# Performance work log

Measured on AMD Instinct MI355X. Metric: run time of the kernel, lower is better.

## Reference

```python
import jax, jax.numpy as jnp
import numpy as np

_EPS = 1e-12      # degenerate-triangle denominator guard
_CHUNK = 64       # triangles processed per scan step


def _bary(p, a, b, c):
    """Barycentric coords of points p w.r.t. triangle (a,b,c). Broadcasts.
    Returns [..., 3] = (u, v, w); -1 everywhere for degenerate triangles."""
    v0 = b - a
    v1 = c - a
    v2 = p - a
    d00 = jnp.sum(v0 * v0, -1)
    d01 = jnp.sum(v0 * v1, -1)
    d11 = jnp.sum(v1 * v1, -1)
    d20 = jnp.sum(v2 * v0, -1)
    d21 = jnp.sum(v2 * v1, -1)
    denom = d00 * d11 - d01 * d01
    bad = jnp.abs(denom) < _EPS
    ds = jnp.where(bad, 1.0, denom)
    v = (d11 * d20 - d01 * d21) / ds
    w = (d00 * d21 - d01 * d20) / ds
    u = 1.0 - v - w
    bar = jnp.stack([u, v, w], -1)
    return jnp.where(bad[..., None], -1.0, bar)


def _pixel_grid(res):
    # pixel-center UVs; x = u along columns, y = v along rows
    t = (jnp.arange(res, dtype=jnp.float32) + 0.5) / res
    gy, gx = jnp.meshgrid(t, t, indexing='ij')
    return jnp.stack([gx, gy], -1)  # [res, res, 2]


def _rasterize_ids(uv, face_indices, res):
    """For each bake pixel, the index of the first (lowest-index) triangle
    containing it, or -1 (== rast[...,-1] in the slang kernel)."""
    px = _pixel_grid(res)                    # [H, W, 2]
    tri = uv[face_indices]                   # [Nf, 3, 2]
    nf = tri.shape[0]
    nchunk = nf // _CHUNK
    tri_c = tri[: nchunk * _CHUNK].reshape(nchunk, _CHUNK, 3, 2)
    fid0 = jnp.full((res, res), -1, dtype=jnp.int32)

    def step(fid, xs):
        ci, tc = xs                          # tc: [C, 3, 2]
        bar = _bary(px[:, :, None, :], tc[:, 0], tc[:, 1], tc[:, 2])  # [H, W, C, 3]
        inside = jnp.all(bar >= 0.0, axis=-1)                          # [H, W, C]
        hit = jnp.any(inside, axis=-1)
        first = jnp.argmax(inside, axis=-1).astype(jnp.int32)          # first hit in chunk
        cand = ci * _CHUNK + first
        fid = jnp.where(hit & (fid < 0), cand, fid)
        return fid, None

    fid, _ = jax.lax.scan(step, fid0, (jnp.arange(nchunk, dtype=jnp.int32), tri_c))
    return fid


def _interpolate(attr, uv, face_indices, fid, res):
    px = _pixel_grid(res)
    tri_idx = face_indices[jnp.clip(fid, 0)]        # [H, W, 3] vertex ids of hit face
    verts = uv[tri_idx]                             # [H, W, 3, 2]
    bar = _bary(px, verts[..., 0, :], verts[..., 1, :], verts[..., 2, :])  # [H, W, 3]
    av = attr[tri_idx]                              # [H, W, 3, 3]
    out = jnp.einsum('hwk,hwkc->hwc', bar, av)
    return jnp.where(fid[..., None] >= 0, out, 0.0)  # zeros outside coverage (kernel inits output to 0)


def setup_inputs() -> dict:
    key = jax.random.key(0)
    k1, k2, k3 = jax.random.split(key, 3)
    Nv, Nf, res = 50000, 512, 512
    attr = jax.random.normal(k1, (Nv, 3), dtype=jnp.float32)
    uv = jax.random.uniform(k2, (Nv, 2), dtype=jnp.float32)
    face_indices = jax.random.randint(k3, (Nf, 3), 0, Nv, dtype=jnp.int32)
    return {"attr": attr, "uv": uv, "face_indices": face_indices, "bake_resolution": res}


def reference(attr, uv, face_indices, bake_resolution):
    fid = _rasterize_ids(uv, face_indices, bake_resolution)
    return _interpolate(attr, uv, face_indices, fid, bake_resolution)
```

## Files before the change

### kernel.cpp

```cpp
#include <hip/hip_runtime.h>
#include <math.h>

#pragma clang fp contract(off)

#define TB_NT   512
#define TB_SLAB 192
#define TS      16

__device__ inline int lanes_below(unsigned long long m) {
    return __builtin_amdgcn_mbcnt_hi((unsigned int)(m >> 32),
           __builtin_amdgcn_mbcnt_lo((unsigned int)m, 0u));
}

__global__ void tb_setup(const float* __restrict__ uv,
                         const int*   __restrict__ fidx,
                         float4* __restrict__ R0, float4* __restrict__ R1,
                         float2* __restrict__ R2, float4* __restrict__ BB,
                         int n_used) {
    int t = blockIdx.x * blockDim.x + threadIdx.x;
    if (t >= n_used) return;
    int i0 = fidx[3 * t + 0];
    int i1 = fidx[3 * t + 1];
    int i2 = fidx[3 * t + 2];
    float ax = uv[2 * i0], ay = uv[2 * i0 + 1];
    float bx = uv[2 * i1], by = uv[2 * i1 + 1];
    float cx = uv[2 * i2], cy = uv[2 * i2 + 1];
    float v0x = bx - ax, v0y = by - ay;
    float v1x = cx - ax, v1y = cy - ay;
    float d00 = v0x * v0x + v0y * v0y;
    float d01 = v0x * v1x + v0y * v1y;
    float d11 = v1x * v1x + v1y * v1y;
    float denom = d00 * d11 - d01 * d01;
    float ds = (fabsf(denom) < 1e-12f) ? 0.0f : denom;
    R0[t] = make_float4(ax, ay, v0x, v0y);
    R1[t] = make_float4(v1x, v1y, d01, ds);
    R2[t] = make_float2(d11, d00);
    if (ds == 0.0f) {
        BB[t] = make_float4(2.0f, -1.0f, 2.0f, -1.0f);
    } else {
        BB[t] = make_float4(fminf(ax, fminf(bx, cx)),
                            fmaxf(ax, fmaxf(bx, cx)),
                            fminf(ay, fminf(by, cy)),
                            fmaxf(ay, fmaxf(by, cy)));
    }
}

__global__ __launch_bounds__(256)
void tb_bake(const float*  __restrict__ attr,
             const int*    __restrict__ fidx,
             const float4* __restrict__ R0, const float4* __restrict__ R1,
             const float2* __restrict__ R2, const float4* __restrict__ BB,
             float* __restrict__ out,
             int res, int n_used, int tiles_x) {
    __shared__ float4         sR0[4][TB_SLAB];
    __shared__ float4         sR1[4][TB_SLAB];
    __shared__ float2         sR2[4][TB_SLAB];
    __shared__ unsigned short sId[4][TB_SLAB];

    int bx = blockIdx.x % tiles_x;
    int by = blockIdx.x / tiles_x;
    int tx = threadIdx.x & (TS - 1);
    int ty = threadIdx.x >> 4;
    int w = bx * TS + tx;
    int h = by * TS + ty;
    bool live = (w < res) && (h < res);
    int pix = h * res + w;
    float pxx = ((float)w + 0.5f) / (float)res;
    float pxy = ((float)h + 0.5f) / (float)res;

    int wv = threadIdx.x >> 6;
    int ln = threadIdx.x & 63;

    float wx0 = (float)(bx * TS) / (float)res;
    float wx1 = (float)(bx * TS + TS) / (float)res;
    float wy0 = (float)(by * TS + wv * 4) / (float)res;
    float wy1 = (float)(by * TS + wv * 4 + 4) / (float)res;

    int   hit = -1;
    float bu = 0.0f, bv = 0.0f, bw = 0.0f;

    for (int base = 0; base < n_used; base += TB_SLAB) {
        if (__all((int)(hit >= 0))) break;
        int nb = min(TB_SLAB, n_used - base);

        int cnt = 0;
        for (int r = 0; r * 64 < nb; ++r) {
            int t = base + r * 64 + ln;
            float4 bb = BB[t];
            float4 r0 = R0[t];
            float4 r1 = R1[t];
            float2 r2 = R2[t];
            bool p = (bb.y >= wx0) && (bb.x <= wx1) &&
                     (bb.w >= wy0) && (bb.z <= wy1);
            unsigned long long m = __ballot((int)p);
            if (p) {
                int idx = cnt + lanes_below(m);
                sR0[wv][idx] = r0;
                sR1[wv][idx] = r1;
                sR2[wv][idx] = r2;
                sId[wv][idx] = (unsigned short)t;
            }
            cnt += __popcll(m);
        }

        for (int i = 0; i < cnt; ++i) {
            float4 qa = sR0[wv][i];
            float4 qb = sR1[wv][i];
            float2 qc = sR2[wv][i];
            float v2x = pxx - qa.x;
            float v2y = pxy - qa.y;
            float d20 = v2x * qa.z + v2y * qa.w;
            float d21 = v2x * qb.x + v2y * qb.y;
            float vn = qc.x * d20 - qb.z * d21;
            float wn = qc.y * d21 - qb.z * d20;
            float ds = qb.w;
            float sg = (ds > 0.0f) ? 1.0f : -1.0f;
            if (hit < 0 && vn * sg >= 0.0f && wn * sg >= 0.0f) {
                float v  = vn / ds;
                float ww = wn / ds;
                float u  = (1.0f - v) - ww;
                if (u >= 0.0f) {
                    bu = u; bv = v; bw = ww;
                    hit = (int)sId[wv][i];
                }
            }
            if (__all((int)(hit >= 0))) break;
        }
    }

    if (live) {
        float o0 = 0.0f, o1 = 0.0f, o2 = 0.0f;
        if (hit >= 0) {
            int i0 = fidx[3 * hit + 0];
            int i1 = fidx[3 * hit + 1];
            int i2 = fidx[3 * hit + 2];
            o0 = (bu * attr[3 * i0 + 0] + bv * attr[3 * i1 + 0]) + bw * attr[3 * i2 + 0];
            o1 = (bu * attr[3 * i0 + 1] + bv * attr[3 * i1 + 1]) + bw * attr[3 * i2 + 1];
            o2 = (bu * attr[3 * i0 + 2] + bv * attr[3 * i1 + 2]) + bw * attr[3 * i2 + 2];
        }
        out[3 * pix + 0] = o0;
        out[3 * pix + 1] = o1;
        out[3 * pix + 2] = o2;
    }
}

extern "C" void kernel_launch(void* const* d_in, const int* in_sizes, int n_in,
                              void* d_out, int out_size, void* d_ws, size_t ws_size,
                              hipStream_t stream) {
    const float* attr = (const float*)d_in[0];
    const float* uv   = (const float*)d_in[1];
    const int*   fidx = (const int*)d_in[2];
    float*       out  = (float*)d_out;

    int res = (int)lround(sqrt((double)(out_size / 3)));
    int nf = in_sizes[2] / 3;
    int n_used = (nf / 64) * 64;

    float4* R0 = (float4*)d_ws;
    float4* R1 = R0 + TB_NT;
    float2* R2 = (float2*)(R1 + TB_NT);
    float4* BB = (float4*)(R2 + TB_NT);

    if (n_used > 0) {
        tb_setup<<<(n_used + 255) / 256, 256, 0, stream>>>(uv, fidx, R0, R1, R2, BB, n_used);
    }
    int tiles_x = (res + TS - 1) / TS;
    int nblocks = tiles_x * tiles_x;
    tb_bake<<<nblocks, 256, 0, stream>>>(attr, fidx, R0, R1, R2, BB,
                                         out, res, n_used, tiles_x);
}
```

Measured before the change: 80.15 us.

## Replace LDS compaction with register readlane broadcast and prefetch next triangle slab

Each wave now keeps one 64-triangle slab in registers, one triangle per lane. It walks the ballot mask of triangles whose bounding box overlaps the wave's 16x4 pixel strip and broadcasts each triangle's parameters with readlane, so shared-memory stores and loads are no longer needed. The next slab's data is prefetched into registers while the current slab is processed. The early-exit condition now also counts dead lanes as finished. This removes LDS traffic and the compaction bookkeeping, but readlane needs scalar registers and serialises work across candidates.

```diff
diff --git a/kernel.cpp b/kernel.cpp
--- a/kernel.cpp
+++ b/kernel.cpp
@@ -3,13 +3,11 @@
 
 #pragma clang fp contract(off)
 
-#define TB_NT   512
-#define TB_SLAB 192
-#define TS      16
+#define TB_NT 512
+#define TS    16
 
-__device__ inline int lanes_below(unsigned long long m) {
-    return __builtin_amdgcn_mbcnt_hi((unsigned int)(m >> 32),
-           __builtin_amdgcn_mbcnt_lo((unsigned int)m, 0u));
+__device__ inline float bcast(float x, int l) {
+    return __int_as_float(__builtin_amdgcn_readlane(__float_as_int(x), l));
 }
 
 __global__ void tb_setup(const float* __restrict__ uv,
@@ -52,11 +50,6 @@
              const float2* __restrict__ R2, const float4* __restrict__ BB,
              float* __restrict__ out,
              int res, int n_used, int tiles_x) {
-    __shared__ float4         sR0[4][TB_SLAB];
-    __shared__ float4         sR1[4][TB_SLAB];
-    __shared__ float2         sR2[4][TB_SLAB];
-    __shared__ unsigned short sId[4][TB_SLAB];
-
     int bx = blockIdx.x % tiles_x;
     int by = blockIdx.x / tiles_x;
     int tx = threadIdx.x & (TS - 1);
@@ -79,41 +72,48 @@
     int   hit = -1;
     float bu = 0.0f, bv = 0.0f, bw = 0.0f;
 
-    for (int base = 0; base < n_used; base += TB_SLAB) {
-        if (__all((int)(hit >= 0))) break;
-        int nb = min(TB_SLAB, n_used - base);
+    int nslab = n_used >> 6;
 
-        int cnt = 0;
-        for (int r = 0; r * 64 < nb; ++r) {
-            int t = base + r * 64 + ln;
-            float4 bb = BB[t];
-            float4 r0 = R0[t];
-            float4 r1 = R1[t];
-            float2 r2 = R2[t];
-            bool p = (bb.y >= wx0) && (bb.x <= wx1) &&
-                     (bb.w >= wy0) && (bb.z <= wy1);
-            unsigned long long m = __ballot((int)p);
-            if (p) {
-                int idx = cnt + lanes_below(m);
-                sR0[wv][idx] = r0;
-                sR1[wv][idx] = r1;
-                sR2[wv][idx] = r2;
-                sId[wv][idx] = (unsigned short)t;
-            }
-            cnt += __popcll(m);
+    float4 cbb = BB[ln];
+    float4 cr0 = R0[ln];
+    float4 cr1 = R1[ln];
+    float2 cr2 = R2[ln];
+
+    for (int s = 0; s < nslab; ++s) {
+        float4 nbb = make_float4(2.0f, -1.0f, 2.0f, -1.0f);
+        float4 nr0 = cr0, nr1 = cr1;
+        float2 nr2 = cr2;
+        if (s + 1 < nslab) {
+            int tn = (s + 1) * 64 + ln;
+            nbb = BB[tn];
+            nr0 = R0[tn];
+            nr1 = R1[tn];
+            nr2 = R2[tn];
         }
 
-        for (int i = 0; i < cnt; ++i) {
-            float4 qa = sR0[wv][i];
-            float4 qb = sR1[wv][i];
-            float2 qc = sR2[wv][i];
-            float v2x = pxx - qa.x;
-            float v2y = pxy - qa.y;
-            float d20 = v2x * qa.z + v2y * qa.w;
-            float d21 = v2x * qb.x + v2y * qb.y;
-            float vn = qc.x * d20 - qb.z * d21;
-            float wn = qc.y * d21 - qb.z * d20;
-            float ds = qb.w;
+        bool p = (cbb.y >= wx0) && (cbb.x <= wx1) &&
+                 (cbb.w >= wy0) && (cbb.z <= wy1);
+        unsigned long long mask = __ballot((int)p);
+
+        while (mask) {
+            int l = (int)__ffsll(mask) - 1;
+            mask &= (mask - 1);
+            float ax  = bcast(cr0.x, l);
+            float ay  = bcast(cr0.y, l);
+            float v0x = bcast(cr0.z, l);
+            float v0y = bcast(cr0.w, l);
+            float v1x = bcast(cr1.x, l);
+            float v1y = bcast(cr1.y, l);
+            float d01 = bcast(cr1.z, l);
+            float ds  = bcast(cr1.w, l);
+            float d11 = bcast(cr2.x, l);
+            float d00 = bcast(cr2.y, l);
+            float v2x = pxx - ax;
+            float v2y = pxy - ay;
+            float d20 = v2x * v0x + v2y * v0y;
+            float d21 = v2x * v1x + v2y * v1y;
+            float vn = d11 * d20 - d01 * d21;
+            float wn = d00 * d21 - d01 * d20;
             float sg = (ds > 0.0f) ? 1.0f : -1.0f;
             if (hit < 0 && vn * sg >= 0.0f && wn * sg >= 0.0f) {
                 float v  = vn / ds;
@@ -121,11 +121,14 @@
                 float u  = (1.0f - v) - ww;
                 if (u >= 0.0f) {
                     bu = u; bv = v; bw = ww;
-                    hit = (int)sId[wv][i];
+                    hit = s * 64 + l;
                 }
             }
-            if (__all((int)(hit >= 0))) break;
+            if (__all((int)(hit >= 0 || !live))) break;
         }
+        if (__all((int)(hit >= 0 || !live))) break;
+
+        cbb = nbb; cr0 = nr0; cr1 = nr1; cr2 = nr2;
     }
 
     if (live) {
```

New measurement: 79.33 us. No clear change (-1.0%).
